# Kernel tuning notes

Hardware: AMD Instinct MI355X
Metric: run time of the kernel (lower is better)

## Reference

```python
import jax, jax.numpy as jnp
import numpy as np


def setup_inputs() -> dict:
    key = jax.random.key(0)
    k1, k2, k3, k4 = jax.random.split(key, 4)
    B, F, E = 8, 64, 50000
    Cout, K = 128, 5
    x = jax.random.normal(k1, (B, F, E), dtype=jnp.float32)
    gemm = jax.random.randint(k2, (B, E, 4), 0, E, dtype=jnp.int64)  # 1-ring neighbor edge indices
    fan_in = F * K
    W = jax.random.normal(k3, (Cout, F, 1, K), dtype=jnp.float32) / np.sqrt(fan_in)
    b = jax.random.normal(k4, (Cout,), dtype=jnp.float32) * 0.01
    return {"x": x, "gemm": gemm, "W": W, "b": b}


def reference(x, gemm, W, b):
    # x: [B, F, E] edge features; gemm: [B, E, 4] neighbor indices in [0, E)
    B, F, E = x.shape
    # pad_gemm prepends the edge's own index as column 0; create_gemm shifts by +1
    # and pads x with a zero column at index 0 (slot for missing / -1 neighbors).
    xp = jnp.concatenate([jnp.zeros((B, F, 1), dtype=x.dtype), x], axis=2)  # [B, F, E+1]
    self_idx = jnp.broadcast_to(jnp.arange(E, dtype=gemm.dtype)[None, :, None], (B, E, 1))
    idx = jnp.concatenate([self_idx, gemm], axis=2) + 1  # [B, E, 5], indices into E+1 slots
    # gather: f[b, f, e, k] = xp[b, f, idx[b, e, k]]
    xp_t = jnp.transpose(xp, (0, 2, 1))  # [B, E+1, F]
    f = jnp.take_along_axis(xp_t, idx.reshape(B, E * 5, 1), axis=1)  # [B, E*5, F]
    f = jnp.transpose(f.reshape(B, E, 5, F), (0, 3, 1, 2))  # [B, F, E, 5]
    # symmetric (order-invariant) pooling over the 4 neighbors
    x0 = f[:, :, :, 0]
    x1 = f[:, :, :, 1] + f[:, :, :, 3]
    x2 = f[:, :, :, 2] + f[:, :, :, 4]
    x3 = jnp.abs(f[:, :, :, 1] - f[:, :, :, 3])
    x4 = jnp.abs(f[:, :, :, 2] - f[:, :, :, 4])
    G = jnp.stack([x0, x1, x2, x3, x4], axis=3)  # [B, F, E, 5]
    # Conv2d with kernel (1, 5) over width-5 map == contraction over (F, 5)
    out = jnp.einsum('bfek,ofk->boe', G, W[:, :, 0, :]) + b[None, :, None]
    return out[..., None]  # [B, Cout, E, 1]
```

## Files before the change

kernel.cpp:

```cpp
#include <hip/hip_runtime.h>
#include <hip/hip_bf16.h>

#define NB 8
#define NF 64
#define NE 50000
#define NO 128
#define NK 320

typedef short short8 __attribute__((ext_vector_type(8)));
typedef float f32x4 __attribute__((ext_vector_type(4)));

__device__ __forceinline__ unsigned short f2bf(float x) {
    union { float f; unsigned int u; } v; v.f = x;
    unsigned int r = v.u + 0x7fffu + ((v.u >> 16) & 1u);
    return (unsigned short)(r >> 16);
}
__device__ __forceinline__ float bf2f(unsigned short h) {
    union { unsigned int u; float f; } v; v.u = ((unsigned int)h) << 16; return v.f;
}

__global__ __launch_bounds__(256) void transpose_x(
    const float* __restrict__ x, unsigned short* __restrict__ xT, int E)
{
    __shared__ float tile[64][65];
    int ntiles = (E + 63) >> 6;
    int b = blockIdx.x / ntiles;
    int t = blockIdx.x % ntiles;
    int e0 = t << 6;
    int le = threadIdx.x & 63;
    int q  = threadIdx.x >> 6;
    const float* xb = x + (size_t)b * NF * E;
    #pragma unroll
    for (int i = 0; i < 16; ++i) {
        int f = q * 16 + i;
        int e = e0 + le;
        tile[f][le] = (e < E) ? xb[(size_t)f * E + e] : 0.0f;
    }
    __syncthreads();
    unsigned short* xTb = xT + (size_t)b * E * NF;
    int fp = (threadIdx.x & 31) * 2;
    int es = threadIdx.x >> 5;
    #pragma unroll
    for (int i = 0; i < 8; ++i) {
        int el = i * 8 + es;
        int e = e0 + el;
        if (e < E) {
            unsigned int pk = (unsigned int)f2bf(tile[fp][el])
                            | ((unsigned int)f2bf(tile[fp + 1][el]) << 16);
            *(unsigned int*)&xTb[(size_t)e * NF + fp] = pk;
        }
    }
}

__global__ __launch_bounds__(256) void prep_w(
    const float* __restrict__ W, unsigned short* __restrict__ Wt)
{
    int idx = blockIdx.x * 256 + threadIdx.x;
    if (idx >= NK * NO) return;
    int K = idx >> 7;
    int o = idx & 127;
    int f  = K & 63;
    int kp = K >> 6;
    float v = W[(size_t)o * (NF * 5) + f * 5 + kp];
    Wt[((size_t)(K >> 3) * NO + o) * 8 + (K & 7)] = f2bf(v);
}

__global__ __launch_bounds__(256) void conv_main(
    const unsigned short* __restrict__ xT,
    const int* __restrict__ gemm,
    const unsigned short* __restrict__ Wt,
    const float* __restrict__ bias,
    float* __restrict__ out,
    int E)
{
    int ntiles = (E + 63) >> 6;
    int b     = blockIdx.x / ntiles;
    int etile = blockIdx.x % ntiles;
    int tid  = threadIdx.x;
    int wave = tid >> 6;
    int lane = tid & 63;
    int l16  = lane & 15;
    int lq   = lane >> 4;

    int e = etile * 64 + wave * 16 + l16;
    bool valid = (e < E);
    int eC = valid ? e : (E - 1);

    int gi[5];
    gi[0] = eC;
    int4 gv = *(const int4*)(gemm + ((size_t)b * E + eC) * 4);
    gi[1] = gv.x; gi[2] = gv.y; gi[3] = gv.z; gi[4] = gv.w;

    f32x4 acc[8];
    #pragma unroll
    for (int mt = 0; mt < 8; ++mt) acc[mt] = (f32x4){0.f, 0.f, 0.f, 0.f};

    const unsigned short* xb = xT + (size_t)b * E * NF;

    #pragma unroll
    for (int half = 0; half < 2; ++half) {
        int f0 = half * 32 + lq * 8;
        uint4 craw[5];
        #pragma unroll
        for (int k = 0; k < 5; ++k)
            craw[k] = *(const uint4*)&xb[(size_t)gi[k] * NF + f0];

        const unsigned short* c1 = (const unsigned short*)&craw[1];
        const unsigned short* c2 = (const unsigned short*)&craw[2];
        const unsigned short* c3 = (const unsigned short*)&craw[3];
        const unsigned short* c4 = (const unsigned short*)&craw[4];

        short8 g[5];
        g[0] = *(short8*)&craw[0];
        unsigned short gb[4][8];
        #pragma unroll
        for (int i = 0; i < 8; ++i) {
            float a1 = bf2f(c1[i]), a2 = bf2f(c2[i]);
            float a3 = bf2f(c3[i]), a4 = bf2f(c4[i]);
            gb[0][i] = f2bf(a1 + a3);
            gb[1][i] = f2bf(a2 + a4);
            gb[2][i] = f2bf(fabsf(a1 - a3));
            gb[3][i] = f2bf(fabsf(a2 - a4));
        }
        g[1] = *(short8*)&gb[0][0];
        g[2] = *(short8*)&gb[1][0];
        g[3] = *(short8*)&gb[2][0];
        g[4] = *(short8*)&gb[3][0];

        #pragma unroll
        for (int kp = 0; kp < 5; ++kp) {
            int ks = kp * 2 + half;
            const unsigned short* wp = Wt + (size_t)(ks * 4 + lq) * NO * 8;
            #pragma unroll
            for (int mt = 0; mt < 8; ++mt) {
                short8 a = *(const short8*)&wp[(mt * 16 + l16) * 8];
                acc[mt] = __builtin_amdgcn_mfma_f32_16x16x32_bf16(a, g[kp], acc[mt], 0, 0, 0);
            }
        }
    }

    if (valid) {
        #pragma unroll
        for (int mt = 0; mt < 8; ++mt) {
            #pragma unroll
            for (int r = 0; r < 4; ++r) {
                int o = mt * 16 + lq * 4 + r;
                out[((size_t)b * NO + o) * E + e] = acc[mt][r] + bias[o];
            }
        }
    }
}

extern "C" void kernel_launch(void* const* d_in, const int* in_sizes, int n_in,
                              void* d_out, int out_size, void* d_ws, size_t ws_size,
                              hipStream_t stream)
{
    const float* x    = (const float*)d_in[0];
    const int*   gemm = (const int*)d_in[1];
    const float* W    = (const float*)d_in[2];
    const float* bias = (const float*)d_in[3];
    float* out = (float*)d_out;

    const int E = NE;
    unsigned short* Wt = (unsigned short*)d_ws;
    unsigned short* xT = (unsigned short*)((char*)d_ws + 131072);

    prep_w<<<(NK * NO + 255) / 256, 256, 0, stream>>>(W, Wt);

    int ntiles = (E + 63) / 64;
    transpose_x<<<NB * ntiles, 256, 0, stream>>>(x, xT, E);

    conv_main<<<NB * ntiles, 256, 0, stream>>>(xT, gemm, Wt, bias, out, E);
}
```

Before: 413.8 us.

## Make conv_main persistent with register-resident weights and LDS-staged gathered features

Result: faster. 372.9 us (-9.9%).

```diff
diff --git a/kernel.cpp b/kernel.cpp
--- a/kernel.cpp
+++ b/kernel.cpp
@@ -6,6 +6,7 @@
 #define NE 50000
 #define NO 128
 #define NK 320
+#define CONV_GRID 768
 
 typedef short short8 __attribute__((ext_vector_type(8)));
 typedef float f32x4 __attribute__((ext_vector_type(4)));
@@ -73,81 +74,122 @@
     float* __restrict__ out,
     int E)
 {
-    int ntiles = (E + 63) >> 6;
-    int b     = blockIdx.x / ntiles;
-    int etile = blockIdx.x % ntiles;
+    __shared__ __align__(16) unsigned short Gs[40 * 64 * 8];
+
     int tid  = threadIdx.x;
     int wave = tid >> 6;
     int lane = tid & 63;
     int l16  = lane & 15;
     int lq   = lane >> 4;
 
-    int e = etile * 64 + wave * 16 + l16;
-    bool valid = (e < E);
-    int eC = valid ? e : (E - 1);
-
-    int gi[5];
-    gi[0] = eC;
-    int4 gv = *(const int4*)(gemm + ((size_t)b * E + eC) * 4);
-    gi[1] = gv.x; gi[2] = gv.y; gi[3] = gv.z; gi[4] = gv.w;
-
-    f32x4 acc[8];
-    #pragma unroll
-    for (int mt = 0; mt < 8; ++mt) acc[mt] = (f32x4){0.f, 0.f, 0.f, 0.f};
-
-    const unsigned short* xb = xT + (size_t)b * E * NF;
-
-    #pragma unroll
-    for (int half = 0; half < 2; ++half) {
-        int f0 = half * 32 + lq * 8;
-        uint4 craw[5];
-        #pragma unroll
-        for (int k = 0; k < 5; ++k)
-            craw[k] = *(const uint4*)&xb[(size_t)gi[k] * NF + f0];
-
-        const unsigned short* c1 = (const unsigned short*)&craw[1];
-        const unsigned short* c2 = (const unsigned short*)&craw[2];
-        const unsigned short* c3 = (const unsigned short*)&craw[3];
-        const unsigned short* c4 = (const unsigned short*)&craw[4];
-
-        short8 g[5];
-        g[0] = *(short8*)&craw[0];
-        unsigned short gb[4][8];
-        #pragma unroll
-        for (int i = 0; i < 8; ++i) {
-            float a1 = bf2f(c1[i]), a2 = bf2f(c2[i]);
-            float a3 = bf2f(c3[i]), a4 = bf2f(c4[i]);
-            gb[0][i] = f2bf(a1 + a3);
-            gb[1][i] = f2bf(a2 + a4);
-            gb[2][i] = f2bf(fabsf(a1 - a3));
-            gb[3][i] = f2bf(fabsf(a2 - a4));
-        }
-        g[1] = *(short8*)&gb[0][0];
-        g[2] = *(short8*)&gb[1][0];
-        g[3] = *(short8*)&gb[2][0];
-        g[4] = *(short8*)&gb[3][0];
-
-        #pragma unroll
-        for (int kp = 0; kp < 5; ++kp) {
-            int ks = kp * 2 + half;
-            const unsigned short* wp = Wt + (size_t)(ks * 4 + lq) * NO * 8;
-            #pragma unroll
-            for (int mt = 0; mt < 8; ++mt) {
-                short8 a = *(const short8*)&wp[(mt * 16 + l16) * 8];
-                acc[mt] = __builtin_amdgcn_mfma_f32_16x16x32_bf16(a, g[kp], acc[mt], 0, 0, 0);
+    short8 wfrag[10][2];
+    #pragma unroll
+    for (int ks = 0; ks < 10; ++ks)
+        #pragma unroll
+        for (int m = 0; m < 2; ++m) {
+            int o = (wave * 2 + m) * 16 + l16;
+            wfrag[ks][m] = *(const short8*)&Wt[((size_t)(ks * 4 + lq) * NO + o) * 8];
+        }
+    float biasr[2][4];
+    #pragma unroll
+    for (int m = 0; m < 2; ++m)
+        #pragma unroll
+        for (int r = 0; r < 4; ++r)
+            biasr[m][r] = bias[(wave * 2 + m) * 16 + lq * 4 + r];
+
+    int ntiles = (E + 63) >> 6;
+    int nunits = NB * ntiles;
+    int ge = tid >> 2;
+    int j  = tid & 3;
+
+    for (int unit = blockIdx.x; unit < nunits; unit += gridDim.x) {
+        int b     = unit / ntiles;
+        int etile = unit % ntiles;
+
+        {
+            int e  = etile * 64 + ge;
+            int eC = (e < E) ? e : (E - 1);
+            const unsigned short* xb = xT + (size_t)b * E * NF;
+            int4 gv = *(const int4*)(gemm + ((size_t)b * E + eC) * 4);
+            int gi[5];
+            gi[0] = eC; gi[1] = gv.x; gi[2] = gv.y; gi[3] = gv.z; gi[4] = gv.w;
+
+            #pragma unroll
+            for (int half = 0; half < 2; ++half) {
+                int f0 = half * 32 + j * 8;
+                uint4 craw[5];
+                #pragma unroll
+                for (int k = 0; k < 5; ++k)
+                    craw[k] = *(const uint4*)&xb[(size_t)gi[k] * NF + f0];
+
+                const unsigned short* c1 = (const unsigned short*)&craw[1];
+                const unsigned short* c2 = (const unsigned short*)&craw[2];
+                const unsigned short* c3 = (const unsigned short*)&craw[3];
+                const unsigned short* c4 = (const unsigned short*)&craw[4];
+
+                uint4 pk[5];
+                pk[0] = craw[0];
+                unsigned short gb[4][8];
+                #pragma unroll
+                for (int i = 0; i < 8; ++i) {
+                    float a1 = bf2f(c1[i]), a2 = bf2f(c2[i]);
+                    float a3 = bf2f(c3[i]), a4 = bf2f(c4[i]);
+                    gb[0][i] = f2bf(a1 + a3);
+                    gb[1][i] = f2bf(a2 + a4);
+                    gb[2][i] = f2bf(fabsf(a1 - a3));
+                    gb[3][i] = f2bf(fabsf(a2 - a4));
+                }
+                pk[1] = *(uint4*)&gb[0][0];
+                pk[2] = *(uint4*)&gb[1][0];
+                pk[3] = *(uint4*)&gb[2][0];
+                pk[4] = *(uint4*)&gb[3][0];
+
+                #pragma unroll
+                for (int kp = 0; kp < 5; ++kp) {
+                    int kblk = kp * 8 + half * 4 + j;
+                    *(uint4*)&Gs[((size_t)kblk * 64 + ge) * 8] = pk[kp];
+                }
             }
         }
-    }
-
-    if (valid) {
-        #pragma unroll
-        for (int mt = 0; mt < 8; ++mt) {
-            #pragma unroll
-            for (int r = 0; r < 4; ++r) {
-                int o = mt * 16 + lq * 4 + r;
-                out[((size_t)b * NO + o) * E + e] = acc[mt][r] + bias[o];
+        __syncthreads();
+
+        f32x4 acc[2][4];
+        #pragma unroll
+        for (int m = 0; m < 2; ++m)
+            #pragma unroll
+            for (int nt = 0; nt < 4; ++nt)
+                acc[m][nt] = (f32x4){0.f, 0.f, 0.f, 0.f};
+
+        #pragma unroll
+        for (int ks = 0; ks < 10; ++ks) {
+            short8 bb[4];
+            #pragma unroll
+            for (int nt = 0; nt < 4; ++nt)
+                bb[nt] = *(const short8*)&Gs[(((size_t)(ks * 4 + lq)) * 64 + nt * 16 + l16) * 8];
+            #pragma unroll
+            for (int m = 0; m < 2; ++m)
+                #pragma unroll
+                for (int nt = 0; nt < 4; ++nt)
+                    acc[m][nt] = __builtin_amdgcn_mfma_f32_16x16x32_bf16(
+                        wfrag[ks][m], bb[nt], acc[m][nt], 0, 0, 0);
+        }
+
+        int e0 = etile * 64;
+        #pragma unroll
+        for (int m = 0; m < 2; ++m) {
+            #pragma unroll
+            for (int nt = 0; nt < 4; ++nt) {
+                int e = e0 + nt * 16 + l16;
+                if (e < E) {
+                    #pragma unroll
+                    for (int r = 0; r < 4; ++r) {
+                        int o = (wave * 2 + m) * 16 + lq * 4 + r;
+                        out[((size_t)b * NO + o) * E + e] = acc[m][nt][r] + biasr[m][r];
+                    }
+                }
             }
         }
+        __syncthreads();
     }
 }
 
@@ -170,5 +212,5 @@
     int ntiles = (E + 63) / 64;
     transpose_x<<<NB * ntiles, 256, 0, stream>>>(x, xT, E);
 
-    conv_main<<<NB * ntiles, 256, 0, stream>>>(xT, gemm, Wt, bias, out, E);
-}
+    conv_main<<<CONV_GRID, 256, 0, stream>>>(xT, gemm, Wt, bias, out, E);
+}
```
